# Kernel optimization log

Measured on AMD Instinct MI355X. Metric: run time of the kernel, lower is better.

The kernel has to match this reference:

```python
import jax, jax.numpy as jnp
import numpy as np

B, LP, LH, D, H = 32, 1024, 1024, 256, 256

def setup_inputs() -> dict:
    key = jax.random.key(0)
    k1, k2, k3 = jax.random.split(key, 3)
    premises = jax.random.normal(k1, (B, LP, D), dtype=jnp.float32)
    hypotheses = jax.random.normal(k2, (B, LH, D), dtype=jnp.float32)
    W_F = jax.random.normal(k3, (D, H), dtype=jnp.float32) * (1.0 / np.sqrt(D))
    return {"premises": premises, "hypotheses": hypotheses, "W_F": W_F}

def reference(premises, hypotheses, W_F):
    # Tanh-projected features: F_p = tanh(P @ W_F), F_h = tanh(H @ W_F)
    F_p = jnp.tanh(jnp.einsum('bpd,dh->bph', premises, W_F))   # [B,LP,H]
    F_h = jnp.tanh(jnp.einsum('bqd,dh->bqh', hypotheses, W_F)) # [B,LH,H]
    # Alignment scores e_ij = F_p . F_h
    eijs = jnp.einsum('bph,bqh->bpq', F_p, F_h)                # [B,LP,LH]
    # betas: for each premise token, softmax over hypothesis tokens, weighted sum of hypotheses
    betas = jnp.einsum('bpq,bqd->bpd', jax.nn.softmax(eijs, axis=-1), hypotheses)  # [B,LP,D]
    # alphas: for each hypothesis token, softmax over premise tokens, weighted sum of premises
    alphas = jnp.einsum('bqp,bpd->bqd',
                        jax.nn.softmax(jnp.swapaxes(eijs, 1, 2), axis=-1),
                        premises)                                                   # [B,LH,D]
    return betas, alphas
```

## Files before the change

### kernel.cpp

```cpp
#include <hip/hip_runtime.h>

typedef _Float16 f16;
typedef __attribute__((ext_vector_type(4))) _Float16 f16x4;
typedef __attribute__((ext_vector_type(8))) _Float16 f16x8;
typedef __attribute__((ext_vector_type(4))) float f32x4;
typedef __attribute__((ext_vector_type(16))) float f32x16;
typedef unsigned int u32;

#define BB 32
#define LL 1024
#define DD 256

#define VMCNT(N) asm volatile("s_waitcnt vmcnt(" #N ")" ::: "memory")
#define LGKMCNT0 asm volatile("s_waitcnt lgkmcnt(0)" ::: "memory")

__device__ __forceinline__ void async_copy16(const f16* g, f16* l) {
  __builtin_amdgcn_global_load_lds(
      (const __attribute__((address_space(1))) u32*)(const void*)g,
      (__attribute__((address_space(3))) u32*)(void*)l, 16, 0, 0);
}

__device__ __forceinline__ u32 pack_pkrtz(float a, float b) {
  auto pk = __builtin_amdgcn_cvt_pkrtz(a, b);
  u32 w;
  __builtin_memcpy(&w, &pk, 4);
  return w;
}

__global__ __launch_bounds__(256) void transpose_to_f16(
    const float* __restrict__ X0, f16* __restrict__ Y0,
    const float* __restrict__ X1, f16* __restrict__ Y1,
    int L, int D, int nbPerInput) {
  __shared__ float T[64][68];
  const int tid = threadIdx.x;
  int bz = blockIdx.z;
  const float* X = X0;
  f16* Y = Y0;
  int b = bz;
  if (bz >= nbPerInput) { X = X1; Y = Y1; b = bz - nbPerInput; }
  const int l0 = blockIdx.x * 64, d0 = blockIdx.y * 64;
  const size_t baseX = (size_t)b * L * D;
#pragma unroll
  for (int pass = 0; pass < 4; ++pass) {
    int r = (tid >> 4) + pass * 16;
    int c = (tid & 15) * 4;
    float4 v = *(const float4*)&X[baseX + (size_t)(l0 + r) * D + d0 + c];
    *(float4*)&T[r][c] = v;
  }
  __syncthreads();
  const size_t baseY = (size_t)b * D * L;
#pragma unroll
  for (int pass = 0; pass < 2; ++pass) {
    int dr = (tid >> 3) + pass * 32;
    int lc = (tid & 7) * 8;
    f16x8 o;
#pragma unroll
    for (int j = 0; j < 8; ++j) o[j] = (f16)T[lc + j][dr];
    *(f16x8*)&Y[baseY + (size_t)(d0 + dr) * L + l0 + lc] = o;
  }
}

__global__ __launch_bounds__(256, 3) void proj_mfma(
    const float* __restrict__ Pin, const float* __restrict__ Hin,
    const f16* __restrict__ Wt, f16* __restrict__ Fp, f16* __restrict__ Fh,
    f16* __restrict__ Vtp, f16* __restrict__ Vth) {
  __shared__ f16 As[64][264];
  const int tid = threadIdx.x;
  const int wv = tid >> 6, lane = tid & 63;
  const int l32 = lane & 31, half = lane >> 5;
  const int wm = wv >> 1, wn = wv & 1;
  const float* A = blockIdx.z ? Hin : Pin;
  f16* F = blockIdx.z ? Fh : Fp;
  f16* VtO = blockIdx.z ? Vth : Vtp;
  const int m0 = blockIdx.x * 64;

  {
    const int r = tid >> 4;
    const int c4 = (tid & 15) * 4;
#pragma unroll
    for (int pp = 0; pp < 4; ++pp)
#pragma unroll
      for (int ch = 0; ch < 4; ++ch) {
        float4 v =
            *(const float4*)&A[(size_t)(m0 + r + pp * 16) * 256 + ch * 64 + c4];
        f16x4 h4;
        h4[0] = (f16)v.x; h4[1] = (f16)v.y; h4[2] = (f16)v.z; h4[3] = (f16)v.w;
        *(f16x4*)&As[r + pp * 16][ch * 64 + c4] = h4;
      }
  }
  __syncthreads();

  f16x8 af[16];
#pragma unroll
  for (int ks = 0; ks < 16; ++ks)
    af[ks] = *(const f16x8*)&As[wm * 32 + l32][ks * 16 + half * 8];

  {
    const int bI = m0 >> 10;
    const int T = ((m0 & 1023) >> 5) + (wv & 1);
    const int dg = (wv >> 1) * 128;
    const int jp = lane & 3;
    const int j = jp ^ ((lane >> 3) & 3);
    const int rloc = (wv & 1) * 32 + j * 8;
#pragma unroll
    for (int e = 0; e < 8; ++e) {
      int d = dg + e * 16 + (lane >> 2);
      f16x8 ov;
#pragma unroll
      for (int jj = 0; jj < 8; ++jj) ov[jj] = As[rloc + jj][d];
      *(f16x8*)&VtO[((size_t)(bI * 32 + T) * 256 + d) * 32 + jp * 8] = ov;
    }
  }
  __syncthreads();

#pragma unroll
  for (int nc = 0; nc < 4; ++nc) {
    f32x16 acc = (f32x16)(0.f);
#pragma unroll
    for (int ks = 0; ks < 16; ++ks) {
      f16x8 wf = *(const f16x8*)&Wt[(size_t)(nc * 64 + wn * 32 + l32) * 256 +
                                    ks * 16 + half * 8];
      acc = __builtin_amdgcn_mfma_f32_32x32x16_f16(af[ks], wf, acc, 0, 0, 0);
    }
#pragma unroll
    for (int r = 0; r < 16; ++r) {
      float xv = acc[r];
      float e2 = __expf(2.f * xv);
      float th = 1.f - 2.f / (e2 + 1.f);
      As[wm * 32 + (r & 3) + 8 * (r >> 2) + 4 * half]
        [nc * 64 + wn * 32 + l32] = (f16)th;
    }
  }
  __syncthreads();

#pragma unroll
  for (int e = 0; e < 8; ++e) {
    int lm = wv * 16 + e * 2 + (lane >> 5);
    int cp = lane & 31;
    int c = cp ^ (lm & 15);
    f16x8 ov = *(const f16x8*)&As[lm][c * 8];
    *(f16x8*)&F[(size_t)(m0 + lm) * 256 + cp * 8] = ov;
  }
}

__global__ __launch_bounds__(256, 2) void flash_mfma(
    const f16* __restrict__ Fpm, const f16* __restrict__ Fhm,
    const f16* __restrict__ Vth, const f16* __restrict__ Vtp,
    float* __restrict__ Out) {
  __shared__ f16 Kb[2][8192];
  __shared__ f16 Vb[2][8192];

  const int tid = threadIdx.x;
  const int wv = tid >> 6, lane = tid & 63;
  const int l32 = lane & 31, half = lane >> 5;

  const f16* Fq = Fpm;
  const f16* Fk = Fhm;
  const f16* Vt = Vth;
  float* O = Out;
  if (blockIdx.y) { Fq = Fhm; Fk = Fpm; Vt = Vtp; O = Out + (size_t)BB * LL * DD; }

  const int x = blockIdx.x;
  const int b = ((x & 7) << 2) | (x >> 6);
  const int p0 = ((x >> 3) & 7) * 128 + wv * 32;
  const int p = p0 + l32;

  const f16* Fq_b = Fq + (size_t)b * LL * DD;
  const f16* Fk_b = Fk + (size_t)b * LL * DD;
  const f16* Vt_b = Vt + (size_t)b * LL * DD;

  f16x8 qf[16];
  {
    const int qsw = p & 15;
#pragma unroll
    for (int s = 0; s < 16; ++s)
      qf[s] = *(const f16x8*)&Fq_b[(size_t)p * DD +
                                   (((2 * s + half) ^ qsw) << 3)];
  }

  float m_run = -1e30f, l_run = 0.f;
  f32x16 o[8];
#pragma unroll
  for (int t = 0; t < 8; ++t) o[t] = (f32x16)(0.f);

  const int ksw = l32 & 15;
  const int vsw = (l32 >> 1) & 3;

  auto stage = [&](int buf, int T) {
#pragma unroll
    for (int ii = 0; ii < 4; ++ii) {
      int i = wv * 4 + ii;
      async_copy16(Fk_b + (size_t)(T * 32 + 2 * i) * DD + lane * 8,
                   &Kb[buf][i * 512]);
    }
#pragma unroll
    for (int ii = 0; ii < 4; ++ii) {
      int i = wv * 4 + ii;
      async_copy16(Vt_b + (size_t)T * 8192 + i * 512 + lane * 8,
                   &Vb[buf][i * 512]);
    }
  };

  auto tile_compute = [&](int cur) {
    f32x16 S0 = (f32x16)(0.f), S1 = (f32x16)(0.f);
    __builtin_amdgcn_s_setprio(1);
#pragma unroll
    for (int s = 0; s < 16; s += 2) {
      f16x8 k0 = *(const f16x8*)&Kb[cur][(l32 << 8) +
                                         (((2 * s + half) ^ ksw) << 3)];
      S0 = __builtin_amdgcn_mfma_f32_32x32x16_f16(k0, qf[s], S0, 0, 0, 0);
      f16x8 k1 = *(const f16x8*)&Kb[cur][(l32 << 8) +
                                         (((2 * s + 2 + half) ^ ksw) << 3)];
      S1 = __builtin_amdgcn_mfma_f32_32x32x16_f16(k1, qf[s + 1], S1, 0, 0, 0);
    }
    __builtin_amdgcn_s_setprio(0);
    f32x16 S;
#pragma unroll
    for (int r = 0; r < 16; ++r) S[r] = S0[r] + S1[r];

    float mt = S[0];
#pragma unroll
    for (int r = 1; r < 16; ++r) mt = fmaxf(mt, S[r]);
    mt = fmaxf(mt, __shfl_xor(mt, 32, 64));

    const bool keep = __all((int)(mt - m_run <= 8.0f)) != 0;
    const float mn = keep ? m_run : fmaxf(m_run, mt);
    float pe[16];
    float ts = 0.f;
#pragma unroll
    for (int r = 0; r < 16; ++r) {
      pe[r] = __expf(S[r] - mn);
      ts += pe[r];
    }
    ts += __shfl_xor(ts, 32, 64);
    if (!keep) {
      const float alpha = __expf(m_run - mn);
      l_run *= alpha;
      m_run = mn;
#pragma unroll
      for (int t = 0; t < 8; ++t)
#pragma unroll
        for (int r = 0; r < 16; ++r) o[t][r] *= alpha;
    }
    l_run += ts;

    u32 pw[8];
#pragma unroll
    for (int i = 0; i < 8; ++i) pw[i] = pack_pkrtz(pe[2 * i], pe[2 * i + 1]);
    u32 rc[4];
    {
      u32 s0 = half ? pw[0] : pw[2];
      u32 s1 = half ? pw[1] : pw[3];
      u32 s2 = half ? pw[4] : pw[6];
      u32 s3 = half ? pw[5] : pw[7];
      rc[0] = (u32)__shfl_xor((int)s0, 32, 64);
      rc[1] = (u32)__shfl_xor((int)s1, 32, 64);
      rc[2] = (u32)__shfl_xor((int)s2, 32, 64);
      rc[3] = (u32)__shfl_xor((int)s3, 32, 64);
    }
    f16x8 pf[2];
#pragma unroll
    for (int h = 0; h < 2; ++h) {
      u32 tmp[4];
      tmp[0] = half ? rc[2 * h] : pw[4 * h];
      tmp[1] = half ? rc[2 * h + 1] : pw[4 * h + 1];
      tmp[2] = half ? pw[4 * h + 2] : rc[2 * h];
      tmp[3] = half ? pw[4 * h + 3] : rc[2 * h + 1];
      __builtin_memcpy(&pf[h], tmp, 16);
    }

    __builtin_amdgcn_s_setprio(1);
#pragma unroll
    for (int t = 0; t < 8; ++t) {
      int vrow = (t * 32 + l32) << 5;
      f16x8 v0 = *(const f16x8*)&Vb[cur][vrow + ((half ^ vsw) << 3)];
      o[t] = __builtin_amdgcn_mfma_f32_32x32x16_f16(v0, pf[0], o[t], 0, 0, 0);
      f16x8 v1 = *(const f16x8*)&Vb[cur][vrow + (((2 + half) ^ vsw) << 3)];
      o[t] = __builtin_amdgcn_mfma_f32_32x32x16_f16(v1, pf[1], o[t], 0, 0, 0);
    }
    __builtin_amdgcn_s_setprio(0);
  };

  stage(0, 0);
  int cur = 0;
  for (int it = 0; it < 31; ++it) {
    stage(cur ^ 1, it + 1);
    VMCNT(8);
    __builtin_amdgcn_sched_barrier(0);
    __builtin_amdgcn_s_barrier();
    tile_compute(cur);
    __builtin_amdgcn_s_barrier();
    cur ^= 1;
  }
  VMCNT(0);
  __builtin_amdgcn_sched_barrier(0);
  __builtin_amdgcn_s_barrier();
  tile_compute(cur);
  __syncthreads();

  const float inv = 1.f / l_run;
  float* Tw = (float*)&Kb[0][0] + wv * (32 * 36);
  float* Ob = O + (size_t)b * LL * DD;
#pragma unroll
  for (int t = 0; t < 8; ++t) {
#pragma unroll
    for (int g = 0; g < 4; ++g) {
      int C = 2 * g + half;
      f32x4 v;
      v[0] = o[t][4 * g + 0] * inv;
      v[1] = o[t][4 * g + 1] * inv;
      v[2] = o[t][4 * g + 2] * inv;
      v[3] = o[t][4 * g + 3] * inv;
      *(f32x4*)&Tw[l32 * 36 + C * 4] = v;
    }
    LGKMCNT0;
#pragma unroll
    for (int pass = 0; pass < 4; ++pass) {
      int row = pass * 8 + (lane >> 3);
      int Cr = lane & 7;
      f32x4 v = *(const f32x4*)&Tw[row * 36 + Cr * 4];
      *(f32x4*)&Ob[(size_t)(p0 + row) * DD + t * 32 + Cr * 4] = v;
    }
    LGKMCNT0;
  }
}

extern "C" void kernel_launch(void* const* d_in, const int* in_sizes, int n_in,
                              void* d_out, int out_size, void* d_ws,
                              size_t ws_size, hipStream_t stream) {
  const float* premises = (const float*)d_in[0];
  const float* hypotheses = (const float*)d_in[1];
  const float* W = (const float*)d_in[2];
  float* out = (float*)d_out;

  const size_t MF = (size_t)BB * LL * DD;
  f16* Fp = (f16*)d_ws;
  f16* Fh = Fp + MF;
  f16* Vth = Fh + MF;
  f16* Vtp = Vth + MF;
  f16* Wt = (f16*)((char*)d_out + (size_t)out_size * 4 - 256 * 256 * 2);

  transpose_to_f16<<<dim3(4, 4, 1), 256, 0, stream>>>(W, Wt, W, Wt, 256, 256, 1);
  proj_mfma<<<dim3(512, 1, 2), 256, 0, stream>>>(premises, hypotheses, Wt, Fp,
                                                 Fh, Vtp, Vth);
  flash_mfma<<<dim3(256, 2), 256, 0, stream>>>(Fp, Fh, Vth, Vtp, out);
}
```

Measured before the change: 241.4 us.

## Store F, V and W in MFMA fragment-ordered layout to drop swizzles

```diff
diff --git a/kernel.cpp b/kernel.cpp
--- a/kernel.cpp
+++ b/kernel.cpp
@@ -27,42 +27,34 @@
   return w;
 }
 
-__global__ __launch_bounds__(256) void transpose_to_f16(
-    const float* __restrict__ X0, f16* __restrict__ Y0,
-    const float* __restrict__ X1, f16* __restrict__ Y1,
-    int L, int D, int nbPerInput) {
-  __shared__ float T[64][68];
+
+__global__ __launch_bounds__(256) void w_to_frag(const float* __restrict__ W,
+                                                 f16* __restrict__ WtF) {
+  __shared__ float T32[256][33];
   const int tid = threadIdx.x;
-  int bz = blockIdx.z;
-  const float* X = X0;
-  f16* Y = Y0;
-  int b = bz;
-  if (bz >= nbPerInput) { X = X1; Y = Y1; b = bz - nbPerInput; }
-  const int l0 = blockIdx.x * 64, d0 = blockIdx.y * 64;
-  const size_t baseX = (size_t)b * L * D;
-#pragma unroll
-  for (int pass = 0; pass < 4; ++pass) {
-    int r = (tid >> 4) + pass * 16;
-    int c = (tid & 15) * 4;
-    float4 v = *(const float4*)&X[baseX + (size_t)(l0 + r) * D + d0 + c];
-    *(float4*)&T[r][c] = v;
-  }
-  __syncthreads();
-  const size_t baseY = (size_t)b * D * L;
-#pragma unroll
-  for (int pass = 0; pass < 2; ++pass) {
-    int dr = (tid >> 3) + pass * 32;
-    int lc = (tid & 7) * 8;
-    f16x8 o;
-#pragma unroll
-    for (int j = 0; j < 8; ++j) o[j] = (f16)T[lc + j][dr];
-    *(f16x8*)&Y[baseY + (size_t)(d0 + dr) * L + l0 + lc] = o;
+  const int N = blockIdx.x;
+  const int nn = tid & 31, kr = tid >> 5;
+#pragma unroll
+  for (int p = 0; p < 32; ++p) {
+    int k = p * 8 + kr;
+    T32[k][nn] = W[(size_t)k * 256 + N * 32 + nn];
+  }
+  __syncthreads();
+  const int wv = tid >> 6, lane = tid & 63;
+  const int l32 = lane & 31, half = lane >> 5;
+#pragma unroll
+  for (int i = 0; i < 4; ++i) {
+    int s = wv * 4 + i;
+    f16x8 ov;
+#pragma unroll
+    for (int j = 0; j < 8; ++j) ov[j] = (f16)T32[s * 16 + half * 8 + j][l32];
+    *(f16x8*)&WtF[(size_t)N * 8192 + s * 512 + lane * 8] = ov;
   }
 }
 
 __global__ __launch_bounds__(256, 3) void proj_mfma(
     const float* __restrict__ Pin, const float* __restrict__ Hin,
-    const f16* __restrict__ Wt, f16* __restrict__ Fp, f16* __restrict__ Fh,
+    const f16* __restrict__ WtF, f16* __restrict__ Fp, f16* __restrict__ Fh,
     f16* __restrict__ Vtp, f16* __restrict__ Vth) {
   __shared__ f16 As[64][264];
   const int tid = threadIdx.x;
@@ -73,6 +65,7 @@
   f16* F = blockIdx.z ? Fh : Fp;
   f16* VtO = blockIdx.z ? Vth : Vtp;
   const int m0 = blockIdx.x * 64;
+  const int T0 = m0 >> 5;
 
   {
     const int r = tid >> 4;
@@ -96,19 +89,18 @@
     af[ks] = *(const f16x8*)&As[wm * 32 + l32][ks * 16 + half * 8];
 
   {
-    const int bI = m0 >> 10;
-    const int T = ((m0 & 1023) >> 5) + (wv & 1);
-    const int dg = (wv >> 1) * 128;
-    const int jp = lane & 3;
-    const int j = jp ^ ((lane >> 3) & 3);
-    const int rloc = (wv & 1) * 32 + j * 8;
-#pragma unroll
-    for (int e = 0; e < 8; ++e) {
-      int d = dg + e * 16 + (lane >> 2);
+#pragma unroll
+    for (int i = 0; i < 8; ++i) {
+      int idx = wv * 8 + i;
+      int Tl = idx >> 4;
+      int t = (idx >> 1) & 7;
+      int qh = idx & 1;
+      int qb = Tl * 32 + qh * 16 + half * 8;
       f16x8 ov;
 #pragma unroll
-      for (int jj = 0; jj < 8; ++jj) ov[jj] = As[rloc + jj][d];
-      *(f16x8*)&VtO[((size_t)(bI * 32 + T) * 256 + d) * 32 + jp * 8] = ov;
+      for (int j = 0; j < 8; ++j) ov[j] = As[qb + j][t * 32 + l32];
+      *(f16x8*)&VtO[(size_t)(T0 + Tl) * 8192 + t * 1024 + qh * 512 +
+                    half * 256 + l32 * 8] = ov;
     }
   }
   __syncthreads();
@@ -118,8 +110,8 @@
     f32x16 acc = (f32x16)(0.f);
 #pragma unroll
     for (int ks = 0; ks < 16; ++ks) {
-      f16x8 wf = *(const f16x8*)&Wt[(size_t)(nc * 64 + wn * 32 + l32) * 256 +
-                                    ks * 16 + half * 8];
+      f16x8 wf = *(const f16x8*)&WtF[(size_t)nc * 16384 + wn * 8192 +
+                                     ks * 512 + lane * 8];
       acc = __builtin_amdgcn_mfma_f32_32x32x16_f16(af[ks], wf, acc, 0, 0, 0);
     }
 #pragma unroll
@@ -134,12 +126,13 @@
   __syncthreads();
 
 #pragma unroll
-  for (int e = 0; e < 8; ++e) {
-    int lm = wv * 16 + e * 2 + (lane >> 5);
-    int cp = lane & 31;
-    int c = cp ^ (lm & 15);
-    f16x8 ov = *(const f16x8*)&As[lm][c * 8];
-    *(f16x8*)&F[(size_t)(m0 + lm) * 256 + cp * 8] = ov;
+  for (int i = 0; i < 8; ++i) {
+    int idx = wv * 8 + i;
+    int Tl = idx >> 4;
+    int s = idx & 15;
+    f16x8 ov = *(const f16x8*)&As[Tl * 32 + l32][s * 16 + half * 8];
+    *(f16x8*)&F[(size_t)(T0 + Tl) * 8192 + s * 512 + half * 256 + l32 * 8] =
+        ov;
   }
 }
 
@@ -171,11 +164,9 @@
 
   f16x8 qf[16];
   {
-    const int qsw = p & 15;
-#pragma unroll
-    for (int s = 0; s < 16; ++s)
-      qf[s] = *(const f16x8*)&Fq_b[(size_t)p * DD +
-                                   (((2 * s + half) ^ qsw) << 3)];
+    const f16* qt = Fq_b + (size_t)(p >> 5) * 8192 + half * 256 + (p & 31) * 8;
+#pragma unroll
+    for (int s = 0; s < 16; ++s) qf[s] = *(const f16x8*)&qt[s * 512];
   }
 
   float m_run = -1e30f, l_run = 0.f;
@@ -183,21 +174,18 @@
 #pragma unroll
   for (int t = 0; t < 8; ++t) o[t] = (f32x16)(0.f);
 
-  const int ksw = l32 & 15;
-  const int vsw = (l32 >> 1) & 3;
-
   auto stage = [&](int buf, int T) {
+    const f16* kt = Fk_b + (size_t)T * 8192;
+    const f16* vt = Vt_b + (size_t)T * 8192;
 #pragma unroll
     for (int ii = 0; ii < 4; ++ii) {
       int i = wv * 4 + ii;
-      async_copy16(Fk_b + (size_t)(T * 32 + 2 * i) * DD + lane * 8,
-                   &Kb[buf][i * 512]);
+      async_copy16(kt + i * 512 + lane * 8, &Kb[buf][i * 512]);
     }
 #pragma unroll
     for (int ii = 0; ii < 4; ++ii) {
       int i = wv * 4 + ii;
-      async_copy16(Vt_b + (size_t)T * 8192 + i * 512 + lane * 8,
-                   &Vb[buf][i * 512]);
+      async_copy16(vt + i * 512 + lane * 8, &Vb[buf][i * 512]);
     }
   };
 
@@ -206,11 +194,9 @@
     __builtin_amdgcn_s_setprio(1);
 #pragma unroll
     for (int s = 0; s < 16; s += 2) {
-      f16x8 k0 = *(const f16x8*)&Kb[cur][(l32 << 8) +
-                                         (((2 * s + half) ^ ksw) << 3)];
+      f16x8 k0 = *(const f16x8*)&Kb[cur][s * 512 + lane * 8];
       S0 = __builtin_amdgcn_mfma_f32_32x32x16_f16(k0, qf[s], S0, 0, 0, 0);
-      f16x8 k1 = *(const f16x8*)&Kb[cur][(l32 << 8) +
-                                         (((2 * s + 2 + half) ^ ksw) << 3)];
+      f16x8 k1 = *(const f16x8*)&Kb[cur][(s + 1) * 512 + lane * 8];
       S1 = __builtin_amdgcn_mfma_f32_32x32x16_f16(k1, qf[s + 1], S1, 0, 0, 0);
     }
     __builtin_amdgcn_s_setprio(0);
@@ -272,10 +258,9 @@
     __builtin_amdgcn_s_setprio(1);
 #pragma unroll
     for (int t = 0; t < 8; ++t) {
-      int vrow = (t * 32 + l32) << 5;
-      f16x8 v0 = *(const f16x8*)&Vb[cur][vrow + ((half ^ vsw) << 3)];
+      f16x8 v0 = *(const f16x8*)&Vb[cur][t * 1024 + lane * 8];
       o[t] = __builtin_amdgcn_mfma_f32_32x32x16_f16(v0, pf[0], o[t], 0, 0, 0);
-      f16x8 v1 = *(const f16x8*)&Vb[cur][vrow + (((2 + half) ^ vsw) << 3)];
+      f16x8 v1 = *(const f16x8*)&Vb[cur][t * 1024 + 512 + lane * 8];
       o[t] = __builtin_amdgcn_mfma_f32_32x32x16_f16(v1, pf[1], o[t], 0, 0, 0);
     }
     __builtin_amdgcn_s_setprio(0);
@@ -338,10 +323,10 @@
   f16* Fh = Fp + MF;
   f16* Vth = Fh + MF;
   f16* Vtp = Vth + MF;
-  f16* Wt = (f16*)((char*)d_out + (size_t)out_size * 4 - 256 * 256 * 2);
-
-  transpose_to_f16<<<dim3(4, 4, 1), 256, 0, stream>>>(W, Wt, W, Wt, 256, 256, 1);
-  proj_mfma<<<dim3(512, 1, 2), 256, 0, stream>>>(premises, hypotheses, Wt, Fp,
+  f16* WtF = (f16*)((char*)d_out + (size_t)out_size * 4 - 256 * 256 * 2);
+
+  w_to_frag<<<dim3(8), 256, 0, stream>>>(W, WtF);
+  proj_mfma<<<dim3(512, 1, 2), 256, 0, stream>>>(premises, hypotheses, WtF, Fp,
                                                  Fh, Vtp, Vth);
   flash_mfma<<<dim3(256, 2), 256, 0, stream>>>(Fp, Fh, Vth, Vtp, out);
 }
```

New measurement: 209.4 us. 13.3% less time.
